# Kernel optimization log

Measured on AMD Instinct MI355X. Metric: run time of the kernel, lower is better.

The kernel has to match this reference:

```python
import jax, jax.numpy as jnp
from jax import lax
import numpy as np

# larq-style ste_sign: forward sign (with sign(0)=+1), straight-through grad clipped to |x|<=1
@jax.custom_vjp
def ste_sign(x):
    return jnp.where(x >= 0, 1.0, -1.0).astype(x.dtype)

def _ste_fwd(x):
    return ste_sign(x), x

def _ste_bwd(x, g):
    return (g * (jnp.abs(x) <= 1.0).astype(g.dtype),)

ste_sign.defvjp(_ste_fwd, _ste_bwd)


def setup_inputs() -> dict:
    key = jax.random.key(0)
    k1, k2 = jax.random.split(key)
    B, H, Wd, Cin = 16, 256, 256, 32
    M, kh, kw, Cout = 4, 3, 3, 32
    x = jax.random.normal(k1, (B, H, Wd, Cin), dtype=jnp.float32)
    W = jax.random.normal(k2, (M, kh, kw, Cin, Cout), dtype=jnp.float32)
    b = jnp.zeros((M, Cout), dtype=jnp.float32)
    return {"x": x, "W": W, "b": b}


def reference(x, W, b):
    # Multibin: sum_{m} QuantConv2D_m(x).  Each branch binarizes the SAME input,
    # so sum of convs == one conv with the sum of the binarized kernels (fused).
    xq = ste_sign(x)                 # [B,H,W,Cin], values in {-1,+1}
    wq = ste_sign(W)                 # [M,kh,kw,Cin,Cout]
    w_sum = wq.sum(axis=0)           # [kh,kw,Cin,Cout]
    y = lax.conv_general_dilated(
        xq, w_sum,
        window_strides=(1, 1),
        padding="SAME",
        dimension_numbers=("NHWC", "HWIO", "NHWC"),
    )
    return y + b.sum(axis=0)         # [B,H,W,Cout]
```

## Files before the change

### kernel.cpp

```cpp
#include <hip/hip_runtime.h>


#define RH      8
#define PITCHB  48
#define PSLOT   (34 * PITCHB)
#define RSLOT   4096
#define RAWOFF  (4 * PSLOT)

typedef __attribute__((ext_vector_type(4)))  int i32x4;
typedef __attribute__((ext_vector_type(16))) int i32x16;

__device__ __forceinline__ void gload16(const void* g, void* l) {
    __builtin_amdgcn_global_load_lds(
        (const __attribute__((address_space(1))) void*)g,
        (__attribute__((address_space(3))) void*)l, 16, 0, 0);
}

__device__ __forceinline__ unsigned packsgn4(uint4 v) {
    unsigned r;
    r  =  (__uint_as_float(v.x) >= 0.0f) ? 0x01u : 0xFFu;
    r |= ((__uint_as_float(v.y) >= 0.0f) ? 0x01u : 0xFFu) << 8;
    r |= ((__uint_as_float(v.z) >= 0.0f) ? 0x01u : 0xFFu) << 16;
    r |= ((__uint_as_float(v.w) >= 0.0f) ? 0x01u : 0xFFu) << 24;
    return r;
}

__global__ void prep_kernel(const float* __restrict__ W, const float* __restrict__ bias,
                            signed char* __restrict__ wsT, float* __restrict__ bsum) {
    int t = blockIdx.x * 256 + threadIdx.x;
    if (t < 9216) {
        int k   = t >> 5;
        int co  = t & 31;
        int tap = k >> 5;
        int ci  = k & 31;
        float s = 0.0f;
        #pragma unroll
        for (int m = 0; m < 4; ++m) {
            float w = W[(m * 9 + tap) * 1024 + ci * 32 + co];
            s += (w >= 0.0f) ? 1.0f : -1.0f;
        }
        wsT[co * 288 + k] = (signed char)(int)s;
    }
    if (t < 32) {
        float s = 0.0f;
        #pragma unroll
        for (int m = 0; m < 4; ++m) s += bias[m * 32 + t];
        bsum[t] = s;
    }
}

#define WAITV(N)                                                                \
    do {                                                                        \
        asm volatile("s_waitcnt vmcnt(" #N ")" ::: "memory");                   \
        __builtin_amdgcn_sched_barrier(0);                                      \
    } while (0)

#define HSEL(J) ((((J) % 3) == 0) ? h0 : ((((J) % 3) == 1) ? h1 : h2))

#define ISSUE_ROW(J, HREG)                                                      \
    do {                                                                        \
        const int row_  = r0 - 1 + (J);                                         \
        const int rowc_ = row_ < 0 ? 0 : (row_ > 255 ? 255 : row_);             \
        const char* gb_ = (const char*)(x + (long)((bimg * 256 + rowc_) * 256   \
                                                   + c0) * 32);                 \
        unsigned char* lb_ = lds + RAWOFF + ((J) % 3) * RSLOT;                  \
        _Pragma("unroll")                                                       \
        for (int k_ = 0; k_ < 4; ++k_)                                          \
            gload16(gb_ + k_ * 1024 + lswz16, lb_ + k_ * 1024);                 \
        HREG = *(x + (long)(bimg * 256 + rowc_) * 8192 + hoff);                 \
        __builtin_amdgcn_sched_barrier(0);                                      \
    } while (0)

#define PACK_ROW(J, HREG)                                                       \
    do {                                                                        \
        const int row_   = r0 - 1 + (J);                                        \
        const bool rowok_ = (row_ >= 0) && (row_ < 256);                        \
        unsigned char* ps_ = lds + ((J) & 3) * PSLOT;                           \
        const unsigned char* rs_ = lds + RAWOFF + ((J) % 3) * RSLOT;            \
        ps_[hpx * PITCHB + (lane & 31)] =                                       \
            (rowok_ && hok) ? ((HREG >= 0.0f) ? 0x01 : 0xFF) : 0;               \
        uint4 o_;                                                               \
        if (rowok_) {                                                           \
            uint4 w0_ = *(const uint4*)(rs_ + (ppx * 8 + ((ph * 4 + 0) ^ pxr)) * 16); \
            uint4 w1_ = *(const uint4*)(rs_ + (ppx * 8 + ((ph * 4 + 1) ^ pxr)) * 16); \
            uint4 w2_ = *(const uint4*)(rs_ + (ppx * 8 + ((ph * 4 + 2) ^ pxr)) * 16); \
            uint4 w3_ = *(const uint4*)(rs_ + (ppx * 8 + ((ph * 4 + 3) ^ pxr)) * 16); \
            o_ = make_uint4(packsgn4(w0_), packsgn4(w1_),                       \
                            packsgn4(w2_), packsgn4(w3_));                      \
        } else {                                                                \
            o_ = make_uint4(0u, 0u, 0u, 0u);                                    \
        }                                                                       \
        *(uint4*)(ps_ + (ppx + 1) * PITCHB + ph * 16) = o_;                     \
    } while (0)

__global__ __launch_bounds__(64, 2) void conv_kernel(const float* __restrict__ x,
                                                     const signed char* __restrict__ wsT,
                                                     const float* __restrict__ bsum,
                                                     float* __restrict__ out) {
    __shared__ __align__(16) unsigned char lds[4 * PSLOT + 3 * RSLOT];

    const int lane = threadIdx.x;
    const int lrow = lane & 31;
    const int lk   = lane >> 5;

    const int bs   = blockIdx.x;
    const int c0   = (bs & 7) * 32;
    const int r0   = ((bs >> 3) & 31) * RH;
    const int bimg = bs >> 8;

    i32x4 bfrag[9];
    #pragma unroll
    for (int t = 0; t < 9; ++t)
        bfrag[t] = *(const i32x4*)(wsT + lrow * 288 + t * 32 + lk * 16);
    const float bsv = bsum[lrow];

    const int lswz16 = (lane ^ ((lane >> 3) & 7)) * 16;
    const int hcol   = (lane < 32) ? (c0 > 0 ? c0 - 1 : 0)
                                   : (c0 + 32 < 256 ? c0 + 32 : 255);
    const bool hok   = (lane < 32) ? (c0 > 0) : (c0 + 32 < 256);
    const int  hpx   = (lane < 32) ? 0 : 33;
    const long hoff  = (long)hcol * 32 + (lane & 31);
    const int  ppx   = lane >> 1;
    const int  ph    = lane & 1;
    const int  pxr   = ppx & 7;

    float h0 = 0.f, h1 = 0.f, h2 = 0.f;

    ISSUE_ROW(0, HSEL(0));
    ISSUE_ROW(1, HSEL(1));
    ISSUE_ROW(2, HSEL(2));
    WAITV(10);  PACK_ROW(0, HSEL(0));
    WAITV(5);   PACK_ROW(1, HSEL(1));
    ISSUE_ROW(3, HSEL(3));
    WAITV(5);   PACK_ROW(2, HSEL(2));

    const int a_off = lrow * PITCHB + lk * 16;

    #pragma unroll
    for (int i = 0; i < RH; ++i) {
        if (i <= RH - 3) ISSUE_ROW(i + 4, HSEL(i + 4));

        if (i == 0)      { WAITV(5);  }
        else if (i == 1) { WAITV(21); }
        else if (i == 2) { WAITV(21); }
        else if (i == 3) { WAITV(21); }
        else if (i == 4) { WAITV(21); }
        else if (i == 5) { WAITV(21); }
        else if (i == 6) { WAITV(16); }
        if (i <= RH - 2) PACK_ROW(i + 3, HSEL(i + 3));

        i32x16 acc = {};
        #pragma unroll
        for (int dh = 0; dh < 3; ++dh) {
            const unsigned char* sb = lds + ((i + dh) & 3) * PSLOT + a_off;
            #pragma unroll
            for (int dw = 0; dw < 3; ++dw) {
                i32x4 a = *(const i32x4*)(sb + dw * PITCHB);
                acc = __builtin_amdgcn_mfma_i32_32x32x32_i8(a, bfrag[dh * 3 + dw],
                                                            acc, 0, 0, 0);
            }
        }

        float* op = out + ((long)((bimg * 256 + (r0 + i)) * 256 + c0)) * 32 + lrow;
        #pragma unroll
        for (int reg = 0; reg < 16; ++reg) {
            int pr = (reg & 3) + 8 * (reg >> 2) + 4 * lk;
            op[pr * 32] = (float)acc[reg] + bsv;
        }
    }
}

extern "C" void kernel_launch(void* const* d_in, const int* in_sizes, int n_in,
                              void* d_out, int out_size, void* d_ws, size_t ws_size,
                              hipStream_t stream) {
    const float* x    = (const float*)d_in[0];
    const float* W    = (const float*)d_in[1];
    const float* bias = (const float*)d_in[2];
    float* out = (float*)d_out;

    signed char* wsT = (signed char*)d_ws;
    float* bsum = (float*)((char*)d_ws + 9216);

    prep_kernel<<<36, 256, 0, stream>>>(W, bias, wsT, bsum);
    conv_kernel<<<4096, 64, 0, stream>>>(x, wsT, bsum, out);
}
```

Before: 249.4 us.

## Transpose MFMA operands for float4 output stores and remap block order

Swaps the A and B operands of the int8 MFMA so each lane's accumulators hold four consecutive output channels of one pixel. This lets the epilogue write four float4 stores per lane instead of sixteen scalar stores strided by 32 floats, and the vmcnt wait thresholds are lowered to match the reduced store count. It also remaps the block index so consecutively launched blocks land on different images and row bands, which may improve spreading across XCDs and caches. The risk is that the hand-tuned vmcnt values must now exactly match the new number of outstanding memory operations.

```diff
diff --git a/kernel.cpp b/kernel.cpp
--- a/kernel.cpp
+++ b/kernel.cpp
@@ -103,7 +103,8 @@
     const int lrow = lane & 31;
     const int lk   = lane >> 5;
 
-    const int bs   = blockIdx.x;
+    const int bid  = blockIdx.x;
+    const int bs   = (bid & 7) * 512 + (bid >> 3);
     const int c0   = (bs & 7) * 32;
     const int r0   = ((bs >> 3) & 31) * RH;
     const int bimg = bs >> 8;
@@ -112,7 +113,10 @@
     #pragma unroll
     for (int t = 0; t < 9; ++t)
         bfrag[t] = *(const i32x4*)(wsT + lrow * 288 + t * 32 + lk * 16);
-    const float bsv = bsum[lrow];
+    const float4 bias0 = *(const float4*)(bsum + 0  + 4 * lk);
+    const float4 bias1 = *(const float4*)(bsum + 8  + 4 * lk);
+    const float4 bias2 = *(const float4*)(bsum + 16 + 4 * lk);
+    const float4 bias3 = *(const float4*)(bsum + 24 + 4 * lk);
 
     const int lswz16 = (lane ^ ((lane >> 3) & 7)) * 16;
     const int hcol   = (lane < 32) ? (c0 > 0 ? c0 - 1 : 0)
@@ -140,13 +144,13 @@
     for (int i = 0; i < RH; ++i) {
         if (i <= RH - 3) ISSUE_ROW(i + 4, HSEL(i + 4));
 
-        if (i == 0)      { WAITV(5);  }
-        else if (i == 1) { WAITV(21); }
-        else if (i == 2) { WAITV(21); }
-        else if (i == 3) { WAITV(21); }
-        else if (i == 4) { WAITV(21); }
-        else if (i == 5) { WAITV(21); }
-        else if (i == 6) { WAITV(16); }
+        if (i == 0)      { WAITV(5); }
+        else if (i == 1) { WAITV(9); }
+        else if (i == 2) { WAITV(9); }
+        else if (i == 3) { WAITV(9); }
+        else if (i == 4) { WAITV(9); }
+        else if (i == 5) { WAITV(9); }
+        else if (i == 6) { WAITV(4); }
         if (i <= RH - 2) PACK_ROW(i + 3, HSEL(i + 3));
 
         i32x16 acc = {};
@@ -156,17 +160,29 @@
             #pragma unroll
             for (int dw = 0; dw < 3; ++dw) {
                 i32x4 a = *(const i32x4*)(sb + dw * PITCHB);
-                acc = __builtin_amdgcn_mfma_i32_32x32x32_i8(a, bfrag[dh * 3 + dw],
-                                                            acc, 0, 0, 0);
+                acc = __builtin_amdgcn_mfma_i32_32x32x32_i8(bfrag[dh * 3 + dw],
+                                                            a, acc, 0, 0, 0);
             }
         }
 
-        float* op = out + ((long)((bimg * 256 + (r0 + i)) * 256 + c0)) * 32 + lrow;
-        #pragma unroll
-        for (int reg = 0; reg < 16; ++reg) {
-            int pr = (reg & 3) + 8 * (reg >> 2) + 4 * lk;
-            op[pr * 32] = (float)acc[reg] + bsv;
-        }
+        float* op = out + ((long)((bimg * 256 + (r0 + i)) * 256 + c0 + lrow)) * 32
+                    + 4 * lk;
+        *(float4*)(op + 0)  = make_float4((float)acc[0]  + bias0.x,
+                                          (float)acc[1]  + bias0.y,
+                                          (float)acc[2]  + bias0.z,
+                                          (float)acc[3]  + bias0.w);
+        *(float4*)(op + 8)  = make_float4((float)acc[4]  + bias1.x,
+                                          (float)acc[5]  + bias1.y,
+                                          (float)acc[6]  + bias1.z,
+                                          (float)acc[7]  + bias1.w);
+        *(float4*)(op + 16) = make_float4((float)acc[8]  + bias2.x,
+                                          (float)acc[9]  + bias2.y,
+                                          (float)acc[10] + bias2.z,
+                                          (float)acc[11] + bias2.w);
+        *(float4*)(op + 24) = make_float4((float)acc[12] + bias3.x,
+                                          (float)acc[13] + bias3.y,
+                                          (float)acc[14] + bias3.z,
+                                          (float)acc[15] + bias3.w);
     }
 }
 
```

Result: slower. 258.7 us (+3.8%).

## Pre-pack input signs to int8 in a separate pass before convolution

Applied to the files above, without the earlier changes.

Adds a pack kernel that binarizes the fp32 input into a padded int8 buffer in workspace (48-byte pixel pitch). A new conv kernel then loads pre-packed rows straight into LDS with fewer loads, needs less LDS, and allows higher occupancy. This replaces the in-kernel sign packing and halo handling. The cost is an extra pass over the full input plus a 48MB intermediate write and read. The new path runs only when the workspace is large enough, otherwise the old fused kernel is used.

```diff
diff --git a/kernel.cpp b/kernel.cpp
--- a/kernel.cpp
+++ b/kernel.cpp
@@ -6,6 +6,11 @@
 #define PSLOT   (34 * PITCHB)
 #define RSLOT   4096
 #define RAWOFF  (4 * PSLOT)
+#define SLOTP   2048
+#define NRING   5
+#define XQOFF   16384
+#define XQSZ    50331648
+#define WSNEED  (XQOFF + XQSZ + 4096)
 
 typedef __attribute__((ext_vector_type(4)))  int i32x4;
 typedef __attribute__((ext_vector_type(16))) int i32x16;
@@ -22,6 +27,15 @@
     r |= ((__uint_as_float(v.y) >= 0.0f) ? 0x01u : 0xFFu) << 8;
     r |= ((__uint_as_float(v.z) >= 0.0f) ? 0x01u : 0xFFu) << 16;
     r |= ((__uint_as_float(v.w) >= 0.0f) ? 0x01u : 0xFFu) << 24;
+    return r;
+}
+
+__device__ __forceinline__ unsigned packsgn4f(float4 v) {
+    unsigned r;
+    r  =  ((v.x >= 0.0f) ? 0x01u : 0xFFu);
+    r |= ((v.y >= 0.0f) ? 0x01u : 0xFFu) << 8;
+    r |= ((v.z >= 0.0f) ? 0x01u : 0xFFu) << 16;
+    r |= ((v.w >= 0.0f) ? 0x01u : 0xFFu) << 24;
     return r;
 }
 
@@ -49,11 +63,117 @@
     }
 }
 
+__global__ __launch_bounds__(256) void pack_kernel(const float* __restrict__ x,
+                                                   unsigned char* __restrict__ xq) {
+    int t = blockIdx.x * 256 + threadIdx.x;
+    #pragma unroll
+    for (int it = 0; it < 4; ++it) {
+        int idx = t + it * 2097152;
+        float4 v = ((const float4*)x)[idx];
+        unsigned r = packsgn4f(v);
+        int px = idx >> 3, u = idx & 7;
+        *(unsigned*)(xq + (long)px * 48 + u * 4) = r;
+    }
+}
+
 #define WAITV(N)                                                                \
     do {                                                                        \
         asm volatile("s_waitcnt vmcnt(" #N ")" ::: "memory");                   \
         __builtin_amdgcn_sched_barrier(0);                                      \
     } while (0)
+
+#define ISSUE_P(J)                                                              \
+    do {                                                                        \
+        const int row_  = r0 - 1 + (J);                                         \
+        const int rowc_ = row_ < 0 ? 0 : (row_ > 255 ? 255 : row_);             \
+        const char* gb_ = (const char*)xq +                                     \
+            ((long)(bimg * 256 + rowc_) * 256 + (c0 - 1)) * 48;                 \
+        unsigned char* lb_ = lds + ((J) % NRING) * SLOTP;                       \
+        gload16(gb_ + lane * 16, lb_);                                          \
+        gload16(gb_ + 1024 + lane * 16, lb_ + 1024);                            \
+        __builtin_amdgcn_sched_barrier(0);                                      \
+    } while (0)
+
+#define COMMIT_P(J)                                                             \
+    do {                                                                        \
+        const int row_   = r0 - 1 + (J);                                        \
+        const bool rowok_ = (row_ >= 0) && (row_ < 256);                        \
+        unsigned char* sl_ = lds + ((J) % NRING) * SLOTP;                       \
+        if (!rowok_) {                                                          \
+            if (lane < 34) {                                                    \
+                *(uint4*)(sl_ + lane * 48)      = zr4;                          \
+                *(uint4*)(sl_ + lane * 48 + 16) = zr4;                          \
+            }                                                                   \
+        } else if (hz_on) {                                                     \
+            *(uint4*)(sl_ + hz_ad) = zr4;                                       \
+        }                                                                       \
+    } while (0)
+
+__global__ __launch_bounds__(64, 4) void conv_packed(const unsigned char* __restrict__ xq,
+                                                     const signed char* __restrict__ wsT,
+                                                     const float* __restrict__ bsum,
+                                                     float* __restrict__ out) {
+    __shared__ __align__(16) unsigned char lds[NRING * SLOTP];
+
+    const int lane = threadIdx.x;
+    const int lrow = lane & 31;
+    const int lk   = lane >> 5;
+
+    const int bs   = blockIdx.x;
+    const int c0   = (bs & 7) * 32;
+    const int r0   = ((bs >> 3) & 31) * RH;
+    const int bimg = bs >> 8;
+
+    i32x4 bfrag[9];
+    #pragma unroll
+    for (int t = 0; t < 9; ++t)
+        bfrag[t] = *(const i32x4*)(wsT + lrow * 288 + t * 32 + lk * 16);
+    const float bsv = bsum[lrow];
+
+    const uint4 zr4 = make_uint4(0u, 0u, 0u, 0u);
+    const bool hz_on = ((c0 == 0) && (lane < 2)) ||
+                       ((c0 == 224) && (lane >= 2) && (lane < 4));
+    const int  hz_ad = (lane < 2) ? lane * 16 : (33 * 48 + (lane - 2) * 16);
+
+    ISSUE_P(0);
+    ISSUE_P(1);
+    ISSUE_P(2);
+    WAITV(4);  COMMIT_P(0);
+    WAITV(2);  COMMIT_P(1);
+    ISSUE_P(3);
+    WAITV(2);  COMMIT_P(2);
+
+    const int a_base = lrow * 48 + lk * 16;
+
+    #pragma unroll
+    for (int i = 0; i < RH; ++i) {
+        if (i <= RH - 3) ISSUE_P(i + 4);
+
+        if (i == 0)      { WAITV(2);  }
+        else if (i <= 5) { WAITV(18); }
+        else if (i == 6) { WAITV(16); }
+        if (i <= RH - 2) COMMIT_P(i + 3);
+
+        i32x16 acc = {};
+        #pragma unroll
+        for (int dh = 0; dh < 3; ++dh) {
+            const unsigned char* sb = lds + ((i + dh) % NRING) * SLOTP;
+            #pragma unroll
+            for (int dw = 0; dw < 3; ++dw) {
+                i32x4 a = *(const i32x4*)(sb + a_base + dw * 48);
+                acc = __builtin_amdgcn_mfma_i32_32x32x32_i8(a, bfrag[dh * 3 + dw],
+                                                            acc, 0, 0, 0);
+            }
+        }
+
+        float* op = out + ((long)((bimg * 256 + (r0 + i)) * 256 + c0)) * 32 + lrow;
+        #pragma unroll
+        for (int reg = 0; reg < 16; ++reg) {
+            int pr = (reg & 3) + 8 * (reg >> 2) + 4 * lk;
+            op[pr * 32] = (float)acc[reg] + bsv;
+        }
+    }
+}
 
 #define HSEL(J) ((((J) % 3) == 0) ? h0 : ((((J) % 3) == 1) ? h1 : h2))
 
@@ -93,10 +213,10 @@
         *(uint4*)(ps_ + (ppx + 1) * PITCHB + ph * 16) = o_;                     \
     } while (0)
 
-__global__ __launch_bounds__(64, 2) void conv_kernel(const float* __restrict__ x,
-                                                     const signed char* __restrict__ wsT,
-                                                     const float* __restrict__ bsum,
-                                                     float* __restrict__ out) {
+__global__ __launch_bounds__(64, 2) void conv_fused(const float* __restrict__ x,
+                                                    const signed char* __restrict__ wsT,
+                                                    const float* __restrict__ bsum,
+                                                    float* __restrict__ out) {
     __shared__ __align__(16) unsigned char lds[4 * PSLOT + 3 * RSLOT];
 
     const int lane = threadIdx.x;
@@ -141,11 +261,7 @@
         if (i <= RH - 3) ISSUE_ROW(i + 4, HSEL(i + 4));
 
         if (i == 0)      { WAITV(5);  }
-        else if (i == 1) { WAITV(21); }
-        else if (i == 2) { WAITV(21); }
-        else if (i == 3) { WAITV(21); }
-        else if (i == 4) { WAITV(21); }
-        else if (i == 5) { WAITV(21); }
+        else if (i <= 5) { WAITV(21); }
         else if (i == 6) { WAITV(16); }
         if (i <= RH - 2) PACK_ROW(i + 3, HSEL(i + 3));
 
@@ -178,9 +294,15 @@
     const float* bias = (const float*)d_in[2];
     float* out = (float*)d_out;
 
-    signed char* wsT = (signed char*)d_ws;
-    float* bsum = (float*)((char*)d_ws + 9216);
+    signed char* wsT  = (signed char*)d_ws;
+    float* bsum       = (float*)((char*)d_ws + 9216);
+    unsigned char* xq = (unsigned char*)d_ws + XQOFF;
 
     prep_kernel<<<36, 256, 0, stream>>>(W, bias, wsT, bsum);
-    conv_kernel<<<4096, 64, 0, stream>>>(x, wsT, bsum, out);
-}
+    if (ws_size >= (size_t)WSNEED) {
+        pack_kernel<<<8192, 256, 0, stream>>>(x, xq);
+        conv_packed<<<4096, 64, 0, stream>>>(xq, wsT, bsum, out);
+    } else {
+        conv_fused<<<4096, 64, 0, stream>>>(x, wsT, bsum, out);
+    }
+}
```

Result: slower. 270.1 us (+8.3%).
